# Optimization experiments

Measured on AMD Instinct MI355X. Metric: run time of the kernel, lower is better.

Reference implementation:

```python
import jax, jax.numpy as jnp
import numpy as np

N = 40000
E = 640000
DIN = 128
H = 128
G = 16
C = 10


def setup_inputs() -> dict:
    key = jax.random.key(0)
    ks = jax.random.split(key, 12)
    x = jax.random.normal(ks[0], (N, DIN), dtype=jnp.float32)
    edge_index = jax.random.randint(ks[1], (2, E), 0, N, dtype=jnp.int64)
    batch = jnp.sort(jax.random.randint(ks[2], (N,), 0, G, dtype=jnp.int64))
    s = 1.0 / np.sqrt(H)
    W_in = jax.random.normal(ks[3], (DIN, H), dtype=jnp.float32) * s
    b_in = jnp.zeros((H,), dtype=jnp.float32)
    W1 = jax.random.normal(ks[4], (H, H), dtype=jnp.float32) * s
    b1 = jnp.zeros((H,), dtype=jnp.float32)
    W2 = jax.random.normal(ks[5], (H, H), dtype=jnp.float32) * s
    b2 = jnp.zeros((H,), dtype=jnp.float32)
    Wf1 = jax.random.normal(ks[6], (H, H // 2), dtype=jnp.float32) * s
    bf1 = jnp.zeros((H // 2,), dtype=jnp.float32)
    Wf2 = jax.random.normal(ks[7], (H // 2, C), dtype=jnp.float32) * (1.0 / np.sqrt(H // 2))
    bf2 = jnp.zeros((C,), dtype=jnp.float32)
    return {"x": x, "edge_index": edge_index, "batch": batch,
            "W_in": W_in, "b_in": b_in, "W1": W1, "b1": b1,
            "W2": W2, "b2": b2, "Wf1": Wf1, "bf1": bf1,
            "Wf2": Wf2, "bf2": bf2}


def _gcn_conv(h, src, dst, deg_inv_sqrt, W, b):
    # h' = D^{-1/2} (A + I) D^{-1/2} (h W) + b  (PyG GCNConv with self-loops)
    hw = h @ W  # [N, H]
    norm = deg_inv_sqrt[src] * deg_inv_sqrt[dst]  # [E]
    agg = jax.ops.segment_sum(hw[src] * norm[:, None], dst, num_segments=N)
    agg = agg + hw * (deg_inv_sqrt * deg_inv_sqrt)[:, None]  # self-loop term
    return agg + b


def reference(x, edge_index, batch, W_in, b_in, W1, b1, W2, b2, Wf1, bf1, Wf2, bf2):
    src, dst = edge_index[0], edge_index[1]
    # degree on target nodes, including self-loop (+1)
    deg = jax.ops.segment_sum(jnp.ones((E,), dtype=x.dtype), dst, num_segments=N) + 1.0
    deg_inv_sqrt = jax.lax.rsqrt(deg)

    h = x @ W_in + b_in
    h = jax.nn.relu(_gcn_conv(h, src, dst, deg_inv_sqrt, W1, b1))  # dropout is identity in eval
    h = jax.nn.relu(_gcn_conv(h, src, dst, deg_inv_sqrt, W2, b2))

    # global mean pool by graph id
    sums = jax.ops.segment_sum(h, batch, num_segments=G)  # [G, H]
    counts = jax.ops.segment_sum(jnp.ones((N,), dtype=h.dtype), batch, num_segments=G)
    pooled = sums / jnp.maximum(counts, 1.0)[:, None]

    out = jax.nn.relu(pooled @ Wf1 + bf1) @ Wf2 + bf2  # [G, C]
    return out
```

## Files before the change

kernel.cpp:

```cpp
#include <hip/hip_runtime.h>
#include <hip/hip_fp16.h>

#define NN 40000
#define EE 640000
#define NCH 157

typedef unsigned int uint;
typedef unsigned short ushort;
typedef __attribute__((ext_vector_type(8))) short short8;
typedef __attribute__((ext_vector_type(4))) float floatx4;

__device__ inline ushort f2bf(float f) {
    uint u = __float_as_uint(f);
    return (ushort)((u + 0x7fffu + ((u >> 16) & 1u)) >> 16);
}
__device__ inline float bf_lo(uint u) { return __uint_as_float(u << 16); }
__device__ inline float bf_hi(uint u) { return __uint_as_float(u & 0xffff0000u); }

__device__ inline int lower_bound_dev(const int* __restrict__ a, int n, int x) {
    int lo = 0, hi = n;
    while (lo < hi) { int m = (lo + hi) >> 1; if (a[m] < x) lo = m + 1; else hi = m; }
    return lo;
}

__global__ __launch_bounds__(256) void histprep_kernel(const int* __restrict__ dst,
                                                       int* __restrict__ counts,
                                                       const float* __restrict__ W_in,
                                                       const float* __restrict__ W1,
                                                       const float* __restrict__ b_in,
                                                       const float* __restrict__ W2,
                                                       const int* __restrict__ batch,
                                                       ushort* __restrict__ Bp1,
                                                       ushort* __restrict__ Bp2,
                                                       float* __restrict__ cvec,
                                                       int* __restrict__ glo) {
    int b = blockIdx.x, t = threadIdx.x;
    if (b < 2500) {
        atomicAdd(&counts[dst[b * 256 + t]], 1);
    } else if (b < 2564) {
        int idx = (b - 2500) * 256 + t;
        int k = idx >> 7, n = idx & 127;
        float s = 0.f;
        for (int j = 0; j < 128; ++j) s = fmaf(W_in[k * 128 + j], W1[j * 128 + n], s);
        Bp1[((size_t)(k >> 3) * 128 + n) * 8 + (k & 7)] = f2bf(s);
    } else if (b < 2628) {
        int idx = (b - 2564) * 256 + t;
        int k = idx >> 7, n = idx & 127;
        Bp2[((size_t)(k >> 3) * 128 + n) * 8 + (k & 7)] = f2bf(W2[idx]);
    } else {
        if (t < 128) {
            float s = 0.f;
            for (int k = 0; k < 128; ++k) s = fmaf(b_in[k], W1[k * 128 + t], s);
            cvec[t] = s;
        } else if (t < 128 + 17) {
            int g = t - 128;
            glo[g] = lower_bound_dev(batch, NN, g);
        }
    }
}

__global__ __launch_bounds__(256) void scan_kernel(const int* __restrict__ counts,
                                                   int* __restrict__ goff,
                                                   int* __restrict__ start,
                                                   int* __restrict__ cursor,
                                                   float* __restrict__ dis, int N) {
    __shared__ int ws[4];
    __shared__ int sbase;
    int t = threadIdx.x, lane = t & 63, wv = t >> 6;
    int idx = blockIdx.x * 256 + t;
    int c = (idx < N) ? counts[idx] : 0;
    int v = c;
    #pragma unroll
    for (int d = 1; d < 64; d <<= 1) {
        int u = __shfl_up(v, d, 64);
        if (lane >= d) v += u;
    }
    if (lane == 63) ws[wv] = v;
    __syncthreads();
    if (t == 0) {
        int total = ws[0] + ws[1] + ws[2] + ws[3];
        sbase = atomicAdd(goff, total);
    }
    __syncthreads();
    int off = sbase;
    for (int j = 0; j < wv; ++j) off += ws[j];
    if (idx < N) {
        int excl = off + v - c;
        start[idx] = excl;
        cursor[idx] = excl;
        dis[idx] = rsqrtf((float)c + 1.0f);
    }
}

template <bool ABF16>
__device__ inline void mm_tile(const void* __restrict__ Av, const ushort* __restrict__ Bpack,
                               ushort* __restrict__ C, int tile, int wv, int lane) {
    int m = lane & 15, q = lane >> 4;
    int row = tile * 64 + wv * 16 + m;

    short8 afr[4];
    if (ABF16) {
        const ushort* A = (const ushort*)Av;
        const ushort* ap = A + (size_t)row * 128 + q * 8;
        #pragma unroll
        for (int k0 = 0; k0 < 4; ++k0) afr[k0] = *(const short8*)(ap + k0 * 32);
    } else {
        const float* A = (const float*)Av;
        const float* ap = A + (size_t)row * 128 + q * 8;
        #pragma unroll
        for (int k0 = 0; k0 < 4; ++k0) {
            float4 f0 = *(const float4*)(ap + k0 * 32);
            float4 f1 = *(const float4*)(ap + k0 * 32 + 4);
            short8 a;
            a[0] = (short)f2bf(f0.x); a[1] = (short)f2bf(f0.y);
            a[2] = (short)f2bf(f0.z); a[3] = (short)f2bf(f0.w);
            a[4] = (short)f2bf(f1.x); a[5] = (short)f2bf(f1.y);
            a[6] = (short)f2bf(f1.z); a[7] = (short)f2bf(f1.w);
            afr[k0] = a;
        }
    }

    floatx4 acc[8];
    #pragma unroll
    for (int nt = 0; nt < 8; ++nt) { floatx4 z = {0.f, 0.f, 0.f, 0.f}; acc[nt] = z; }

    #pragma unroll
    for (int nt = 0; nt < 8; ++nt) {
        #pragma unroll
        for (int k0 = 0; k0 < 4; ++k0) {
            short8 bfrag = *(const short8*)(Bpack + ((size_t)(k0 * 4 + q) * 128 + nt * 16 + m) * 8);
            acc[nt] = __builtin_amdgcn_mfma_f32_16x16x32_bf16(afr[k0], bfrag, acc[nt], 0, 0, 0);
        }
    }

    int orow_base = tile * 64 + wv * 16 + q * 4;
    #pragma unroll
    for (int nt = 0; nt < 8; ++nt) {
        #pragma unroll
        for (int r = 0; r < 4; ++r)
            C[(size_t)(orow_base + r) * 128 + nt * 16 + m] = f2bf(acc[nt][r]);
    }
}

__global__ __launch_bounds__(256) void fillmm1_kernel(const int* __restrict__ src,
                                                      const int* __restrict__ dst,
                                                      const float* __restrict__ dis,
                                                      int* __restrict__ cursor,
                                                      uint* __restrict__ edata,
                                                      const float* __restrict__ x,
                                                      const ushort* __restrict__ Bp1,
                                                      ushort* __restrict__ bufA) {
    int b = blockIdx.x, t = threadIdx.x;
    if (b < 2500) {
        int e = b * 256 + t;
        int s = src[e], d = dst[e];
        int pos = atomicAdd(&cursor[d], 1);
        float nrm = dis[s] * dis[d];
        uint pk = (uint)s | ((uint)__half_as_ushort(__float2half_rn(nrm)) << 16);
        edata[pos] = pk;
    } else {
        mm_tile<false>(x, Bp1, bufA, b - 2500, t >> 6, t & 63);
    }
}

__global__ __launch_bounds__(256) void mm2_kernel(const ushort* __restrict__ A,
                                                  const ushort* __restrict__ Bp2,
                                                  ushort* __restrict__ C) {
    mm_tile<true>(A, Bp2, C, blockIdx.x, threadIdx.x >> 6, threadIdx.x & 63);
}

__global__ __launch_bounds__(256) void agg_kernel(const ushort* __restrict__ hw,
                                                  const float* __restrict__ dis,
                                                  const int* __restrict__ start,
                                                  const int* __restrict__ counts,
                                                  const uint* __restrict__ edata,
                                                  const float* __restrict__ cvec,
                                                  const float* __restrict__ bias,
                                                  ushort* __restrict__ out, int N) {
    __shared__ uint eds[4][64];
    int wv = threadIdx.x >> 6;
    int lane = threadIdx.x & 63;
    int q = lane & 15, h4 = lane >> 4;
    int i = blockIdx.x * 4 + wv;
    if (i >= N) return;
    int beg = start[i];
    int deg = counts[i];
    int dmain = deg > 64 ? 64 : deg;
    const uint4* __restrict__ hv4 = (const uint4*)hw;

    uint ed;
    if (lane < dmain) ed = edata[beg + lane];
    else ed = (uint)i;
    eds[wv][lane] = ed;

    float a0 = 0.f, a1 = 0.f, a2 = 0.f, a3 = 0.f;
    float a4 = 0.f, a5 = 0.f, a6 = 0.f, a7 = 0.f;
    float sn = 0.f;

    int dpad = (dmain + 15) & ~15;
    for (int j = 0; j < dpad; j += 16) {
        uint e0 = eds[wv][j + h4];
        uint e1 = eds[wv][j + 4 + h4];
        uint e2 = eds[wv][j + 8 + h4];
        uint e3 = eds[wv][j + 12 + h4];
        uint4 u0 = hv4[(size_t)(e0 & 0xffffu) * 16 + q];
        uint4 u1 = hv4[(size_t)(e1 & 0xffffu) * 16 + q];
        uint4 u2 = hv4[(size_t)(e2 & 0xffffu) * 16 + q];
        uint4 u3 = hv4[(size_t)(e3 & 0xffffu) * 16 + q];
        float n0 = __half2float(__ushort_as_half((ushort)(e0 >> 16)));
        float n1 = __half2float(__ushort_as_half((ushort)(e1 >> 16)));
        float n2 = __half2float(__ushort_as_half((ushort)(e2 >> 16)));
        float n3 = __half2float(__ushort_as_half((ushort)(e3 >> 16)));
        a0 = fmaf(n0, bf_lo(u0.x), a0); a1 = fmaf(n0, bf_hi(u0.x), a1);
        a2 = fmaf(n0, bf_lo(u0.y), a2); a3 = fmaf(n0, bf_hi(u0.y), a3);
        a4 = fmaf(n0, bf_lo(u0.z), a4); a5 = fmaf(n0, bf_hi(u0.z), a5);
        a6 = fmaf(n0, bf_lo(u0.w), a6); a7 = fmaf(n0, bf_hi(u0.w), a7);
        a0 = fmaf(n1, bf_lo(u1.x), a0); a1 = fmaf(n1, bf_hi(u1.x), a1);
        a2 = fmaf(n1, bf_lo(u1.y), a2); a3 = fmaf(n1, bf_hi(u1.y), a3);
        a4 = fmaf(n1, bf_lo(u1.z), a4); a5 = fmaf(n1, bf_hi(u1.z), a5);
        a6 = fmaf(n1, bf_lo(u1.w), a6); a7 = fmaf(n1, bf_hi(u1.w), a7);
        a0 = fmaf(n2, bf_lo(u2.x), a0); a1 = fmaf(n2, bf_hi(u2.x), a1);
        a2 = fmaf(n2, bf_lo(u2.y), a2); a3 = fmaf(n2, bf_hi(u2.y), a3);
        a4 = fmaf(n2, bf_lo(u2.z), a4); a5 = fmaf(n2, bf_hi(u2.z), a5);
        a6 = fmaf(n2, bf_lo(u2.w), a6); a7 = fmaf(n2, bf_hi(u2.w), a7);
        a0 = fmaf(n3, bf_lo(u3.x), a0); a1 = fmaf(n3, bf_hi(u3.x), a1);
        a2 = fmaf(n3, bf_lo(u3.y), a2); a3 = fmaf(n3, bf_hi(u3.y), a3);
        a4 = fmaf(n3, bf_lo(u3.z), a4); a5 = fmaf(n3, bf_hi(u3.z), a5);
        a6 = fmaf(n3, bf_lo(u3.w), a6); a7 = fmaf(n3, bf_hi(u3.w), a7);
        sn += (n0 + n1) + (n2 + n3);
    }
    for (int e = beg + 64; e < beg + deg; ++e) {
        uint et = edata[e];
        if (h4 == 0) {
            float n0 = __half2float(__ushort_as_half((ushort)(et >> 16)));
            uint4 u = hv4[(size_t)(et & 0xffffu) * 16 + q];
            a0 = fmaf(n0, bf_lo(u.x), a0); a1 = fmaf(n0, bf_hi(u.x), a1);
            a2 = fmaf(n0, bf_lo(u.y), a2); a3 = fmaf(n0, bf_hi(u.y), a3);
            a4 = fmaf(n0, bf_lo(u.z), a4); a5 = fmaf(n0, bf_hi(u.z), a5);
            a6 = fmaf(n0, bf_lo(u.w), a6); a7 = fmaf(n0, bf_hi(u.w), a7);
            sn += n0;
        }
    }

    a0 += __shfl_xor(a0, 16); a0 += __shfl_xor(a0, 32);
    a1 += __shfl_xor(a1, 16); a1 += __shfl_xor(a1, 32);
    a2 += __shfl_xor(a2, 16); a2 += __shfl_xor(a2, 32);
    a3 += __shfl_xor(a3, 16); a3 += __shfl_xor(a3, 32);
    a4 += __shfl_xor(a4, 16); a4 += __shfl_xor(a4, 32);
    a5 += __shfl_xor(a5, 16); a5 += __shfl_xor(a5, 32);
    a6 += __shfl_xor(a6, 16); a6 += __shfl_xor(a6, 32);
    a7 += __shfl_xor(a7, 16); a7 += __shfl_xor(a7, 32);
    sn += __shfl_xor(sn, 16); sn += __shfl_xor(sn, 32);

    float di = dis[i];
    float sii = di * di;
    uint4 su = hv4[(size_t)i * 16 + q];
    a0 = fmaf(sii, bf_lo(su.x), a0); a1 = fmaf(sii, bf_hi(su.x), a1);
    a2 = fmaf(sii, bf_lo(su.y), a2); a3 = fmaf(sii, bf_hi(su.y), a3);
    a4 = fmaf(sii, bf_lo(su.z), a4); a5 = fmaf(sii, bf_hi(su.z), a5);
    a6 = fmaf(sii, bf_lo(su.w), a6); a7 = fmaf(sii, bf_hi(su.w), a7);
    sn += sii;

    float c0 = 0.f, c1 = 0.f, c2 = 0.f, c3 = 0.f;
    float c4 = 0.f, c5 = 0.f, c6 = 0.f, c7 = 0.f;
    if (cvec) {
        float4 ca = *(const float4*)(cvec + 8 * q);
        float4 cb = *(const float4*)(cvec + 8 * q + 4);
        c0 = ca.x; c1 = ca.y; c2 = ca.z; c3 = ca.w;
        c4 = cb.x; c5 = cb.y; c6 = cb.z; c7 = cb.w;
    }
    float4 ba = *(const float4*)(bias + 8 * q);
    float4 bb = *(const float4*)(bias + 8 * q + 4);
    float o0 = fmaxf(fmaf(sn, c0, a0) + ba.x, 0.f);
    float o1 = fmaxf(fmaf(sn, c1, a1) + ba.y, 0.f);
    float o2 = fmaxf(fmaf(sn, c2, a2) + ba.z, 0.f);
    float o3 = fmaxf(fmaf(sn, c3, a3) + ba.w, 0.f);
    float o4 = fmaxf(fmaf(sn, c4, a4) + bb.x, 0.f);
    float o5 = fmaxf(fmaf(sn, c5, a5) + bb.y, 0.f);
    float o6 = fmaxf(fmaf(sn, c6, a6) + bb.z, 0.f);
    float o7 = fmaxf(fmaf(sn, c7, a7) + bb.w, 0.f);
    if (h4 == 0) {
        uint4 o;
        o.x = (uint)f2bf(o0) | ((uint)f2bf(o1) << 16);
        o.y = (uint)f2bf(o2) | ((uint)f2bf(o3) << 16);
        o.z = (uint)f2bf(o4) | ((uint)f2bf(o5) << 16);
        o.w = (uint)f2bf(o6) | ((uint)f2bf(o7) << 16);
        ((uint4*)out)[(size_t)i * 16 + q] = o;
    }
}

__global__ __launch_bounds__(256) void poolfinal_kernel(const ushort* __restrict__ h,
                                                        const int* __restrict__ glo,
                                                        float* __restrict__ pools,
                                                        int* __restrict__ ticket,
                                                        const float* __restrict__ Wf1,
                                                        const float* __restrict__ bf1,
                                                        const float* __restrict__ Wf2,
                                                        const float* __restrict__ bf2,
                                                        float* __restrict__ out) {
    __shared__ float pooled[16][128];
    __shared__ float z[16][64];
    __shared__ int slast;
    int t = threadIdx.x, c2 = t & 63, wv = t >> 6;
    int b = blockIdx.x;
    int g = b >> 3, ch = b & 7;
    int lo = glo[g], hi = glo[g + 1];
    int span = hi - lo;
    int chunk = (span + 7) >> 3;
    int r0 = lo + ch * chunk;
    int r1 = hi < r0 + chunk ? hi : r0 + chunk;
    const uint* __restrict__ hv = (const uint*)h;

    float a0 = 0.f, a1 = 0.f;
    #pragma unroll 4
    for (int j = r0 + wv; j < r1; j += 4) {
        uint u = hv[(size_t)j * 64 + c2];
        a0 += bf_lo(u);
        a1 += bf_hi(u);
    }
    if (r0 < r1) {
        atomicAdd(&pools[g * 128 + 2 * c2], a0);
        atomicAdd(&pools[g * 128 + 2 * c2 + 1], a1);
    }

    __syncthreads();
    __threadfence();
    if (t == 0) slast = atomicAdd(ticket, 1);
    __syncthreads();
    if (slast != 127) return;

    for (int idx = t; idx < 2048; idx += 256) {
        int gg = idx >> 7, c = idx & 127;
        int cn = glo[gg + 1] - glo[gg];
        float cnf = (float)(cn > 1 ? cn : 1);
        float ps = __hip_atomic_load(&pools[idx], __ATOMIC_RELAXED, __HIP_MEMORY_SCOPE_AGENT);
        pooled[gg][c] = ps / cnf;
    }
    __syncthreads();
    for (int idx = t; idx < 1024; idx += 256) {
        int gg = idx >> 6, j = idx & 63;
        float s = bf1[j];
        for (int k = 0; k < 128; ++k) s = fmaf(pooled[gg][k], Wf1[k * 64 + j], s);
        z[gg][j] = fmaxf(s, 0.f);
    }
    __syncthreads();
    if (t < 160) {
        int gg = t / 10, k = t % 10;
        float s = bf2[k];
        for (int j = 0; j < 64; ++j) s = fmaf(z[gg][j], Wf2[j * 10 + k], s);
        out[t] = s;
    }
}


extern "C" void kernel_launch(void* const* d_in, const int* in_sizes, int n_in,
                              void* d_out, int out_size, void* d_ws, size_t ws_size,
                              hipStream_t stream) {
    const float* x    = (const float*)d_in[0];
    const int* edge   = (const int*)d_in[1];
    const int* batch  = (const int*)d_in[2];
    const float* W_in = (const float*)d_in[3];
    const float* b_in = (const float*)d_in[4];
    const float* W1   = (const float*)d_in[5];
    const float* b1   = (const float*)d_in[6];
    const float* W2   = (const float*)d_in[7];
    const float* b2   = (const float*)d_in[8];
    const float* Wf1  = (const float*)d_in[9];
    const float* bf1  = (const float*)d_in[10];
    const float* Wf2  = (const float*)d_in[11];
    const float* bf2  = (const float*)d_in[12];
    float* out = (float*)d_out;

    char* ws = (char*)d_ws;
    size_t off = 0;
    auto alloc = [&](size_t bytes) -> void* {
        void* p = ws + off;
        off += (bytes + 511) & ~(size_t)511;
        return p;
    };
    int* counts   = (int*)alloc((size_t)NN * 4);
    float* pools  = (float*)alloc(16 * 128 * 4);
    int* misc     = (int*)alloc(512);
    size_t zero_bytes = off;
    int* goff     = misc;
    int* ticket   = misc + 1;
    int* glo      = misc + 8;
    ushort* bufA  = (ushort*)alloc((size_t)NN * 128 * 2);
    ushort* bufB  = (ushort*)alloc((size_t)NN * 128 * 2);
    ushort* Bp1   = (ushort*)alloc(128 * 128 * 2);
    ushort* Bp2   = (ushort*)alloc(128 * 128 * 2);
    float* cvec   = (float*)alloc(128 * 4);
    float* dis    = (float*)alloc((size_t)NN * 4);
    int* start    = (int*)alloc((size_t)NN * 4);
    int* cursor   = (int*)alloc((size_t)NN * 4);
    uint* edata   = (uint*)alloc((size_t)EE * 4);

    hipMemsetAsync(counts, 0, zero_bytes, stream);

    histprep_kernel<<<2629, 256, 0, stream>>>(edge + EE, counts, W_in, W1, b_in, W2,
                                              batch, Bp1, Bp2, cvec, glo);
    scan_kernel<<<NCH, 256, 0, stream>>>(counts, goff, start, cursor, dis, NN);
    fillmm1_kernel<<<2500 + NN / 64, 256, 0, stream>>>(edge, edge + EE, dis, cursor,
                                                       edata, x, Bp1, bufA);
    agg_kernel<<<NN / 4, 256, 0, stream>>>(bufA, dis, start, counts, edata, cvec, b1, bufB, NN);
    mm2_kernel<<<NN / 64, 256, 0, stream>>>(bufB, Bp2, bufA);
    agg_kernel<<<NN / 4, 256, 0, stream>>>(bufA, dis, start, counts, edata, nullptr, b2, bufB, NN);
    poolfinal_kernel<<<128, 256, 0, stream>>>(bufB, glo, pools, ticket,
                                              Wf1, bf1, Wf2, bf2, out);
}
```

Measured before the change: 240.3 us.

## Fuse first aggregation with second GEMM via shared-memory tile

```diff
diff --git a/kernel.cpp b/kernel.cpp
--- a/kernel.cpp
+++ b/kernel.cpp
@@ -9,6 +9,7 @@
 typedef unsigned short ushort;
 typedef __attribute__((ext_vector_type(8))) short short8;
 typedef __attribute__((ext_vector_type(4))) float floatx4;
+typedef __attribute__((ext_vector_type(4))) uint uint4e;
 
 __device__ inline ushort f2bf(float f) {
     uint u = __float_as_uint(f);
@@ -163,10 +164,158 @@
     }
 }
 
-__global__ __launch_bounds__(256) void mm2_kernel(const ushort* __restrict__ A,
-                                                  const ushort* __restrict__ Bp2,
-                                                  ushort* __restrict__ C) {
-    mm_tile<true>(A, Bp2, C, blockIdx.x, threadIdx.x >> 6, threadIdx.x & 63);
+__global__ __launch_bounds__(512) void agg1m_kernel(const ushort* __restrict__ hw,
+                                                    const float* __restrict__ dis,
+                                                    const int* __restrict__ start,
+                                                    const int* __restrict__ counts,
+                                                    const uint* __restrict__ edata,
+                                                    const float* __restrict__ cvec,
+                                                    const float* __restrict__ bias,
+                                                    const ushort* __restrict__ Bp2,
+                                                    ushort* __restrict__ C) {
+    __shared__ ushort Atile[64][128];
+    __shared__ uint eds[8][64];
+    int t = threadIdx.x;
+    int wv = t >> 6, lane = t & 63;
+    int qg = lane & 15, h4 = lane >> 4;
+    const uint4* __restrict__ hv4 = (const uint4*)hw;
+    int base = blockIdx.x * 64;
+    char* abase = (char*)&Atile[0][0];
+
+    for (int n = 0; n < 8; ++n) {
+        int nl = wv * 8 + n;
+        int i = base + nl;
+        int beg = start[i];
+        int deg = counts[i];
+        int dmain = deg > 64 ? 64 : deg;
+
+        uint ed;
+        if (lane < dmain) ed = edata[beg + lane];
+        else ed = (uint)i;
+        eds[wv][lane] = ed;
+
+        float a0 = 0.f, a1 = 0.f, a2 = 0.f, a3 = 0.f;
+        float a4 = 0.f, a5 = 0.f, a6 = 0.f, a7 = 0.f;
+        float sn = 0.f;
+
+        int dpad = (dmain + 15) & ~15;
+        for (int j = 0; j < dpad; j += 16) {
+            uint e0 = eds[wv][j + h4];
+            uint e1 = eds[wv][j + 4 + h4];
+            uint e2 = eds[wv][j + 8 + h4];
+            uint e3 = eds[wv][j + 12 + h4];
+            uint4 u0 = hv4[(size_t)(e0 & 0xffffu) * 16 + qg];
+            uint4 u1 = hv4[(size_t)(e1 & 0xffffu) * 16 + qg];
+            uint4 u2 = hv4[(size_t)(e2 & 0xffffu) * 16 + qg];
+            uint4 u3 = hv4[(size_t)(e3 & 0xffffu) * 16 + qg];
+            float n0 = __half2float(__ushort_as_half((ushort)(e0 >> 16)));
+            float n1 = __half2float(__ushort_as_half((ushort)(e1 >> 16)));
+            float n2 = __half2float(__ushort_as_half((ushort)(e2 >> 16)));
+            float n3 = __half2float(__ushort_as_half((ushort)(e3 >> 16)));
+            a0 = fmaf(n0, bf_lo(u0.x), a0); a1 = fmaf(n0, bf_hi(u0.x), a1);
+            a2 = fmaf(n0, bf_lo(u0.y), a2); a3 = fmaf(n0, bf_hi(u0.y), a3);
+            a4 = fmaf(n0, bf_lo(u0.z), a4); a5 = fmaf(n0, bf_hi(u0.z), a5);
+            a6 = fmaf(n0, bf_lo(u0.w), a6); a7 = fmaf(n0, bf_hi(u0.w), a7);
+            a0 = fmaf(n1, bf_lo(u1.x), a0); a1 = fmaf(n1, bf_hi(u1.x), a1);
+            a2 = fmaf(n1, bf_lo(u1.y), a2); a3 = fmaf(n1, bf_hi(u1.y), a3);
+            a4 = fmaf(n1, bf_lo(u1.z), a4); a5 = fmaf(n1, bf_hi(u1.z), a5);
+            a6 = fmaf(n1, bf_lo(u1.w), a6); a7 = fmaf(n1, bf_hi(u1.w), a7);
+            a0 = fmaf(n2, bf_lo(u2.x), a0); a1 = fmaf(n2, bf_hi(u2.x), a1);
+            a2 = fmaf(n2, bf_lo(u2.y), a2); a3 = fmaf(n2, bf_hi(u2.y), a3);
+            a4 = fmaf(n2, bf_lo(u2.z), a4); a5 = fmaf(n2, bf_hi(u2.z), a5);
+            a6 = fmaf(n2, bf_lo(u2.w), a6); a7 = fmaf(n2, bf_hi(u2.w), a7);
+            a0 = fmaf(n3, bf_lo(u3.x), a0); a1 = fmaf(n3, bf_hi(u3.x), a1);
+            a2 = fmaf(n3, bf_lo(u3.y), a2); a3 = fmaf(n3, bf_hi(u3.y), a3);
+            a4 = fmaf(n3, bf_lo(u3.z), a4); a5 = fmaf(n3, bf_hi(u3.z), a5);
+            a6 = fmaf(n3, bf_lo(u3.w), a6); a7 = fmaf(n3, bf_hi(u3.w), a7);
+            sn += (n0 + n1) + (n2 + n3);
+        }
+        for (int e = beg + 64; e < beg + deg; ++e) {
+            uint et = edata[e];
+            if (h4 == 0) {
+                float n0 = __half2float(__ushort_as_half((ushort)(et >> 16)));
+                uint4 u = hv4[(size_t)(et & 0xffffu) * 16 + qg];
+                a0 = fmaf(n0, bf_lo(u.x), a0); a1 = fmaf(n0, bf_hi(u.x), a1);
+                a2 = fmaf(n0, bf_lo(u.y), a2); a3 = fmaf(n0, bf_hi(u.y), a3);
+                a4 = fmaf(n0, bf_lo(u.z), a4); a5 = fmaf(n0, bf_hi(u.z), a5);
+                a6 = fmaf(n0, bf_lo(u.w), a6); a7 = fmaf(n0, bf_hi(u.w), a7);
+                sn += n0;
+            }
+        }
+
+        a0 += __shfl_xor(a0, 16); a0 += __shfl_xor(a0, 32);
+        a1 += __shfl_xor(a1, 16); a1 += __shfl_xor(a1, 32);
+        a2 += __shfl_xor(a2, 16); a2 += __shfl_xor(a2, 32);
+        a3 += __shfl_xor(a3, 16); a3 += __shfl_xor(a3, 32);
+        a4 += __shfl_xor(a4, 16); a4 += __shfl_xor(a4, 32);
+        a5 += __shfl_xor(a5, 16); a5 += __shfl_xor(a5, 32);
+        a6 += __shfl_xor(a6, 16); a6 += __shfl_xor(a6, 32);
+        a7 += __shfl_xor(a7, 16); a7 += __shfl_xor(a7, 32);
+        sn += __shfl_xor(sn, 16); sn += __shfl_xor(sn, 32);
+
+        float di = dis[i];
+        float sii = di * di;
+        uint4 su = hv4[(size_t)i * 16 + qg];
+        a0 = fmaf(sii, bf_lo(su.x), a0); a1 = fmaf(sii, bf_hi(su.x), a1);
+        a2 = fmaf(sii, bf_lo(su.y), a2); a3 = fmaf(sii, bf_hi(su.y), a3);
+        a4 = fmaf(sii, bf_lo(su.z), a4); a5 = fmaf(sii, bf_hi(su.z), a5);
+        a6 = fmaf(sii, bf_lo(su.w), a6); a7 = fmaf(sii, bf_hi(su.w), a7);
+        sn += sii;
+
+        float4 ca = *(const float4*)(cvec + 8 * qg);
+        float4 cb = *(const float4*)(cvec + 8 * qg + 4);
+        float4 ba = *(const float4*)(bias + 8 * qg);
+        float4 bb = *(const float4*)(bias + 8 * qg + 4);
+        float o0 = fmaxf(fmaf(sn, ca.x, a0) + ba.x, 0.f);
+        float o1 = fmaxf(fmaf(sn, ca.y, a1) + ba.y, 0.f);
+        float o2 = fmaxf(fmaf(sn, ca.z, a2) + ba.z, 0.f);
+        float o3 = fmaxf(fmaf(sn, ca.w, a3) + ba.w, 0.f);
+        float o4 = fmaxf(fmaf(sn, cb.x, a4) + bb.x, 0.f);
+        float o5 = fmaxf(fmaf(sn, cb.y, a5) + bb.y, 0.f);
+        float o6 = fmaxf(fmaf(sn, cb.z, a6) + bb.z, 0.f);
+        float o7 = fmaxf(fmaf(sn, cb.w, a7) + bb.w, 0.f);
+
+        if (h4 == 0) {
+            uint4e o;
+            o.x = (uint)f2bf(o0) | ((uint)f2bf(o1) << 16);
+            o.y = (uint)f2bf(o2) | ((uint)f2bf(o3) << 16);
+            o.z = (uint)f2bf(o4) | ((uint)f2bf(o5) << 16);
+            o.w = (uint)f2bf(o6) | ((uint)f2bf(o7) << 16);
+            int slot = qg ^ (nl & 7);
+            *(uint4e*)(abase + nl * 256 + slot * 16) = o;
+        }
+    }
+
+    __syncthreads();
+
+    if (wv < 4) {
+        int m = lane & 15, qm = lane >> 4;
+        int row = wv * 16 + m;
+        short8 afr[4];
+        #pragma unroll
+        for (int k0 = 0; k0 < 4; ++k0) {
+            int slot = (qm + 4 * k0) ^ (row & 7);
+            afr[k0] = *(const short8*)(abase + row * 256 + slot * 16);
+        }
+        floatx4 acc[8];
+        #pragma unroll
+        for (int nt = 0; nt < 8; ++nt) { floatx4 z = {0.f, 0.f, 0.f, 0.f}; acc[nt] = z; }
+        #pragma unroll
+        for (int nt = 0; nt < 8; ++nt) {
+            #pragma unroll
+            for (int k0 = 0; k0 < 4; ++k0) {
+                short8 bfrag = *(const short8*)(Bp2 + ((size_t)(k0 * 4 + qm) * 128 + nt * 16 + m) * 8);
+                acc[nt] = __builtin_amdgcn_mfma_f32_16x16x32_bf16(afr[k0], bfrag, acc[nt], 0, 0, 0);
+            }
+        }
+        int orow_base = base + wv * 16 + qm * 4;
+        #pragma unroll
+        for (int nt = 0; nt < 8; ++nt) {
+            #pragma unroll
+            for (int r = 0; r < 4; ++r)
+                C[(size_t)(orow_base + r) * 128 + nt * 16 + m] = f2bf(acc[nt][r]);
+        }
+    }
 }
 
 __global__ __launch_bounds__(256) void agg_kernel(const ushort* __restrict__ hw,
@@ -387,6 +536,7 @@
     int* glo      = misc + 8;
     ushort* bufA  = (ushort*)alloc((size_t)NN * 128 * 2);
     ushort* bufB  = (ushort*)alloc((size_t)NN * 128 * 2);
+    ushort* bufC  = (ushort*)alloc((size_t)NN * 128 * 2);
     ushort* Bp1   = (ushort*)alloc(128 * 128 * 2);
     ushort* Bp2   = (ushort*)alloc(128 * 128 * 2);
     float* cvec   = (float*)alloc(128 * 4);
@@ -402,9 +552,9 @@
     scan_kernel<<<NCH, 256, 0, stream>>>(counts, goff, start, cursor, dis, NN);
     fillmm1_kernel<<<2500 + NN / 64, 256, 0, stream>>>(edge, edge + EE, dis, cursor,
                                                        edata, x, Bp1, bufA);
-    agg_kernel<<<NN / 4, 256, 0, stream>>>(bufA, dis, start, counts, edata, cvec, b1, bufB, NN);
-    mm2_kernel<<<NN / 64, 256, 0, stream>>>(bufB, Bp2, bufA);
-    agg_kernel<<<NN / 4, 256, 0, stream>>>(bufA, dis, start, counts, edata, nullptr, b2, bufB, NN);
+    agg1m_kernel<<<NN / 64, 512, 0, stream>>>(bufA, dis, start, counts, edata,
+                                              cvec, b1, Bp2, bufC);
+    agg_kernel<<<NN / 4, 256, 0, stream>>>(bufC, dis, start, counts, edata, nullptr, b2, bufB, NN);
     poolfinal_kernel<<<128, 256, 0, stream>>>(bufB, glo, pools, ticket,
                                               Wf1, bf1, Wf2, bf2, out);
 }
```

Result: slower. 250.3 us (+4.2%).
